# Performance work log

Hardware: AMD Instinct MI355X
Metric: run time of the kernel (lower is better)

The kernel has to match this reference:

```python
import jax, jax.numpy as jnp
import numpy as np

IN_DIM = 128
OUT_DIM = 128
D_MODEL = IN_DIM // 4        # mamba d_model = 32
D_STATE = 16
D_CONV = 4
EXPAND = 2
D_INNER = EXPAND * D_MODEL   # 64
DT_RANK = (D_MODEL + 15) // 16  # ceil(d_model/16) = 2
N_MIXERS = 3                 # shared + 2 experts (stacked on leading axis)
B, DD, HH, WW = 2, 16, 16, 16


def setup_inputs() -> dict:
    key = jax.random.key(0)
    ks = jax.random.split(key, 12)
    rn = lambda k, s, sc=0.05: jax.random.normal(k, s, dtype=jnp.float32) * sc
    M = N_MIXERS
    return {
        "x": jax.random.normal(ks[0], (B, IN_DIM, DD, HH, WW), dtype=jnp.float32),
        "dataset_id": jax.random.randint(ks[1], (B,), 0, 2),
        "ln_g": jnp.ones((M, IN_DIM), jnp.float32),
        "ln_b": jnp.zeros((M, IN_DIM), jnp.float32),
        "in_w": rn(ks[2], (M, 2 * D_INNER, D_MODEL)),
        "conv_w": rn(ks[3], (M, D_INNER, D_CONV), 0.2),
        "conv_b": rn(ks[4], (M, D_INNER), 0.1),
        "xp_w": rn(ks[5], (M, DT_RANK + 2 * D_STATE, D_INNER)),
        "dt_w": rn(ks[6], (M, D_INNER, DT_RANK), 0.2),
        "dt_b": rn(ks[7], (M, D_INNER), 0.1),
        "A_log": jnp.broadcast_to(jnp.log(jnp.arange(1, D_STATE + 1, dtype=jnp.float32)), (M, D_INNER, D_STATE)) + jnp.zeros((M, D_INNER, D_STATE), jnp.float32),
        "Dp": jnp.ones((M, D_INNER), jnp.float32),
        "out_w": rn(ks[8], (M, D_MODEL, D_INNER)),
        "proj_w": rn(ks[9], (M, OUT_DIM, IN_DIM)),
        "proj_b": jnp.zeros((M, OUT_DIM), jnp.float32),
        "skip": jnp.ones((M,), jnp.float32),
    }


def layernorm(x, g, b, eps=1e-5):
    mu = jnp.mean(x, -1, keepdims=True)
    var = jnp.mean((x - mu) ** 2, -1, keepdims=True)
    return (x - mu) * jax.lax.rsqrt(var + eps) * g + b


def mamba(xp, p):
    # Standard Mamba block: in_proj -> causal depthwise conv1d -> selective scan -> SiLU gate -> out_proj
    # xp: (B, L, d_model)
    Bb, L, _ = xp.shape
    xz = jnp.einsum('bld,ed->ble', xp, p["in_w"])            # (B,L,2*d_inner)
    xi, z = jnp.split(xz, 2, axis=-1)
    conv = jax.lax.conv_general_dilated(xi.transpose(0, 2, 1), p["conv_w"][:, None, :], (1,), [(D_CONV - 1, 0)], feature_group_count=D_INNER)
    xi = jax.nn.silu(conv + p["conv_b"][None, :, None]).transpose(0, 2, 1)  # (B,L,d_inner)
    dbc = jnp.einsum('bld,ed->ble', xi, p["xp_w"])
    dt_low = dbc[..., :DT_RANK]
    Bm = dbc[..., DT_RANK:DT_RANK + D_STATE]
    Cm = dbc[..., DT_RANK + D_STATE:]
    delta = jax.nn.softplus(jnp.einsum('blr,dr->bld', dt_low, p["dt_w"]) + p["dt_b"])  # (B,L,d_inner)
    A = -jnp.exp(p["A_log"])                                  # (d_inner, d_state)

    def step(h, inp):
        xt, dt, Bt, Ct = inp                                  # (B,di),(B,di),(B,ds),(B,ds)
        dA = jnp.exp(dt[..., None] * A)                       # (B,d_inner,d_state)
        h = dA * h + (dt * xt)[..., None] * Bt[:, None, :]
        return h, jnp.einsum('bds,bs->bd', h, Ct)

    h0 = jnp.zeros((Bb, D_INNER, D_STATE), xp.dtype)
    xs = (xi.transpose(1, 0, 2), delta.transpose(1, 0, 2), Bm.transpose(1, 0, 2), Cm.transpose(1, 0, 2))
    _, ys = jax.lax.scan(step, h0, xs)
    y = ys.transpose(1, 0, 2) + p["Dp"] * xi
    y = y * jax.nn.silu(z)
    return jnp.einsum('ble,de->bld', y, p["out_w"])


def mixer(x, p):
    # PetaloMixer pom_module='full': LN -> 4-way channel chunk -> shared Mamba + skip -> concat -> LN -> Linear
    Bb, C, Dd, Hh, Ww = x.shape
    L = Dd * Hh * Ww
    xf = x.reshape(Bb, C, L).transpose(0, 2, 1)               # (B,L,C)
    xn = layernorm(xf, p["ln_g"], p["ln_b"])
    parts = jnp.stack(jnp.split(xn, 4, axis=-1), 0)           # (4,B,L,d_model)
    outs = jax.vmap(lambda q: mamba(q, p))(parts) + p["skip"] * parts
    xm = jnp.concatenate([outs[i] for i in range(4)], -1)     # (B,L,C)
    xm = layernorm(xm, p["ln_g"], p["ln_b"])                  # same LayerNorm reused, as in torch code
    xpj = jnp.einsum('blc,oc->blo', xm, p["proj_w"]) + p["proj_b"]
    return xpj.transpose(0, 2, 1).reshape(Bb, OUT_DIM, Dd, Hh, Ww)


def _forward(x, dataset_id, params):
    shared = mixer(x, {k: v[0] for k, v in params.items()})
    # experts: compute both over full batch (vectorized), then per-sample select by dataset_id
    eouts = jax.vmap(lambda p: mixer(x, p))({k: v[1:] for k, v in params.items()})  # (2,B,out,D,H,W)
    ids = jnp.minimum(dataset_id, N_MIXERS - 2)               # clamp: min(m, n_experts-1)
    expert_out = eouts[ids, jnp.arange(x.shape[0])]
    return shared + expert_out                                # Dropout3d(p=0.2) is identity in eval mode


def reference(x, dataset_id, ln_g, ln_b, in_w, conv_w, conv_b, xp_w, dt_w, dt_b, A_log, Dp, out_w, proj_w, proj_b, skip):
    params = dict(ln_g=ln_g, ln_b=ln_b, in_w=in_w, conv_w=conv_w, conv_b=conv_b, xp_w=xp_w, dt_w=dt_w, dt_b=dt_b, A_log=A_log, Dp=Dp, out_w=out_w, proj_w=proj_w, proj_b=proj_b, skip=skip)
    return _forward(x, dataset_id, params)
```

## Files before the change

### kernel.cpp

```cpp
#include <hip/hip_runtime.h>
#include <math.h>

#define LSEQ 4096
#define CIN  128
#define DI   64
#define NS   16
#define NP   4
#define NJ   4
#define NSEQ 16
#define NC   128
#define LC   32
#define LOG2E 1.44269504f
#define LN2   0.6931471806f

__device__ __forceinline__ int mixer_of(const int* did, int j){
  if((j&1)==0) return 0;
  int d = did[j>>1];
  return 1 + (d < 1 ? d : 1);
}
__device__ __forceinline__ float fexp2(float x){ return __builtin_amdgcn_exp2f(x); }
__device__ __forceinline__ float silu_f(float x){
  return x*__builtin_amdgcn_rcpf(1.f + fexp2(-x*LOG2E));
}
__device__ __forceinline__ float softplus_f(float x){
  return x>20.f ? x : LN2*__builtin_amdgcn_logf(1.f + fexp2(x*LOG2E));
}

__global__ __launch_bounds__(256) void k12_fused(
  const float* __restrict__ x, const int* __restrict__ did,
  const float* __restrict__ ln_g, const float* __restrict__ ln_b,
  const float* __restrict__ in_w,
  const float* __restrict__ conv_w, const float* __restrict__ conv_b,
  const float* __restrict__ xp_w, const float* __restrict__ dt_w, const float* __restrict__ dt_b,
  const float* __restrict__ A_log,
  float* __restrict__ xnb, float* __restrict__ zb, float* __restrict__ dxb,
  float* __restrict__ bmb, float* __restrict__ cmb,
  float* __restrict__ pb, float* __restrict__ eb)
{
  const int seq = blockIdx.y, j = seq>>2, q = seq&3, b = j>>1;
  const int chunk = blockIdx.x, l0 = chunk*32;
  const int m = mixer_of(did, j);
  const int t = threadIdx.x, d = t&63, r = t>>6;

  __shared__ float s_x[36*132];
  __shared__ float s_xn[36][36];
  __shared__ float s_xzf[35][64];
  __shared__ float s_bS[32][16];
  __shared__ float s_dbc[32][2];
  __shared__ float s_cwT[4][64];
  __shared__ float s_xpw01[2][64];
  __shared__ float s_cb[64], s_dtw[128], s_dtb[64];
  __shared__ float s_mu[36], s_rs[36];
  float* s_xi = s_x;
  float* s_dl = s_x + 2048;

  for(int idx=t; idx<1152; idx+=256){
    int c = idx/9, f = idx - c*9;
    int l = l0 - 4 + f*4;
    float4 v;
    if(l >= 0) v = *(const float4*)(x + ((size_t)b*CIN + c)*LSEQ + l);
    else       v = make_float4(0.f,0.f,0.f,0.f);
    s_x[(f*4+0)*132 + c] = v.x;
    s_x[(f*4+1)*132 + c] = v.y;
    s_x[(f*4+2)*132 + c] = v.z;
    s_x[(f*4+3)*132 + c] = v.w;
  }
  float wreg_in[32];
  {
    const float4* wp = (const float4*)(in_w + (size_t)m*4096 + (size_t)(t&127)*32);
    #pragma unroll
    for(int i=0;i<8;i++){
      float4 v = wp[i];
      wreg_in[i*4+0]=v.x; wreg_in[i*4+1]=v.y; wreg_in[i*4+2]=v.z; wreg_in[i*4+3]=v.w;
    }
  }
  { int k=t>>6, dd=t&63; s_cwT[k][dd]=conv_w[m*256+dd*4+k]; }
  if(t<64){ s_cb[t]=conv_b[m*64+t]; s_dtb[t]=dt_b[m*64+t]; }
  if(t<128){ s_dtw[t]=dt_w[m*128+t]; s_xpw01[t>>6][t&63]=xp_w[m*2176 + t]; }
  __syncthreads();

  {
    const int lane=t&63, g=lane&7, lw=lane>>3;
    {
      int row = r*8 + lw;
      const float4* xr4 = (const float4*)(s_x + row*132 + g*16);
      float sum=0.f, vs=0.f;
      #pragma unroll
      for(int k=0;k<4;k++){
        float4 v = xr4[k];
        sum += (v.x+v.y)+(v.z+v.w);
        vs  += v.x*v.x + v.y*v.y + v.z*v.z + v.w*v.w;
      }
      sum += __shfl_xor(sum,1); vs += __shfl_xor(vs,1);
      sum += __shfl_xor(sum,2); vs += __shfl_xor(vs,2);
      sum += __shfl_xor(sum,4); vs += __shfl_xor(vs,4);
      float mu  = sum*(1.f/128.f);
      float var = fmaxf(vs*(1.f/128.f) - mu*mu, 0.f);
      if(g==0){ s_mu[row]=mu; s_rs[row]=rsqrtf(var+1e-5f); }
    }
    if(r==0 && lw<4){
      int row = 32 + lw;
      const float4* xr4 = (const float4*)(s_x + row*132 + g*16);
      float sum=0.f, vs=0.f;
      #pragma unroll
      for(int k=0;k<4;k++){
        float4 v = xr4[k];
        sum += (v.x+v.y)+(v.z+v.w);
        vs  += v.x*v.x + v.y*v.y + v.z*v.z + v.w*v.w;
      }
      sum += __shfl_xor(sum,1); vs += __shfl_xor(vs,1);
      sum += __shfl_xor(sum,2); vs += __shfl_xor(vs,2);
      sum += __shfl_xor(sum,4); vs += __shfl_xor(vs,4);
      float mu  = sum*(1.f/128.f);
      float var = fmaxf(vs*(1.f/128.f) - mu*mu, 0.f);
      if(g==0){ s_mu[row]=mu; s_rs[row]=rsqrtf(var+1e-5f); }
    }
  }
  __syncthreads();

  for(int idx=t; idx<1120; idx+=256){
    int row = (idx>>5) + 1, cc = idx&31;
    float xv = s_x[row*132 + q*32 + cc];
    float xn = (xv - s_mu[row])*s_rs[row]*ln_g[m*128 + q*32+cc] + ln_b[m*128 + q*32+cc];
    s_xn[row][cc] = xn;
    if(row>=4) xnb[((size_t)j*LSEQ + l0+row-4)*128 + q*32+cc] = xn;
  }
  __syncthreads();

  {
    const int e = t&127, hh = t>>7;
    if(e < 64){
      int r0 = 1 + hh*18, r1 = hh ? 36 : 19;
      for(int row=r0; row<r1; ++row){
        const float4* xr4 = (const float4*)(&s_xn[row][0]);
        float acc=0.f;
        #pragma unroll
        for(int k4=0;k4<8;k4++){
          float4 xv = xr4[k4];
          acc += xv.x*wreg_in[k4*4+0] + xv.y*wreg_in[k4*4+1]
               + xv.z*wreg_in[k4*4+2] + xv.w*wreg_in[k4*4+3];
        }
        if(chunk==0 && row<4) acc = 0.f;
        s_xzf[row-1][e] = acc;
      }
    } else {
      int r0 = 4 + hh*16, r1 = r0 + 16;
      for(int row=r0; row<r1; ++row){
        const float4* xr4 = (const float4*)(&s_xn[row][0]);
        float acc=0.f;
        #pragma unroll
        for(int k4=0;k4<8;k4++){
          float4 xv = xr4[k4];
          acc += xv.x*wreg_in[k4*4+0] + xv.y*wreg_in[k4*4+1]
               + xv.z*wreg_in[k4*4+2] + xv.w*wreg_in[k4*4+3];
        }
        zb[((size_t)seq*LSEQ + l0+row-4)*64 + (e-64)] = acc;
      }
    }
  }
  const int o2 = t&31, rg = t>>5;
  float wreg[64];
  {
    const float4* wp = (const float4*)(xp_w + (size_t)m*2176 + (size_t)(2+o2)*64);
    #pragma unroll
    for(int k4=0;k4<16;k4++){
      float4 v = wp[k4];
      wreg[k4*4+0]=v.x; wreg[k4*4+1]=v.y; wreg[k4*4+2]=v.z; wreg[k4*4+3]=v.w;
    }
  }
  __syncthreads();

  float xir[8];
  {
    float lz[11];
    #pragma unroll
    for(int i=0;i<11;i++) lz[i] = s_xzf[r*8+i][d];
    float cw0=s_cwT[0][d], cw1=s_cwT[1][d], cw2=s_cwT[2][d], cw3=s_cwT[3][d], cb=s_cb[d];
    #pragma unroll
    for(int i=0;i<8;i++){
      float xc = cb + lz[i]*cw0 + lz[i+1]*cw1 + lz[i+2]*cw2 + lz[i+3]*cw3;
      xir[i] = silu_f(xc);
      s_xi[(r*8+i)*64 + d] = xir[i];
    }
  }

  {
    float pr[8];
    #pragma unroll
    for(int i=0;i<8;i++){
      float p0 = xir[i]*s_xpw01[0][d];
      float p1 = xir[i]*s_xpw01[1][d];
      float q0 = p0 + __shfl_xor(p0,1);
      float q1 = p1 + __shfl_xor(p1,1);
      pr[i] = (d&1) ? q1 : q0;
    }
    #pragma unroll
    for(int off=2; off<64; off<<=1){
      #pragma unroll
      for(int i=0;i<8;i++) pr[i] += __shfl_xor(pr[i], off);
    }
    if(d<2){
      #pragma unroll
      for(int i=0;i<8;i++) s_dbc[r*8+i][d] = pr[i];
    }
  }
  __syncthreads();

  {
    float w0=s_dtw[d*2], w1=s_dtw[d*2+1], bb=s_dtb[d];
    #pragma unroll
    for(int i=0;i<8;i++){
      int ll=r*8+i;
      float dtv = s_dbc[ll][0]*w0 + s_dbc[ll][1]*w1 + bb;
      float dlv = softplus_f(dtv);
      s_dl[ll*64 + d] = dlv;
      *(float2*)(dxb + ((size_t)seq*LSEQ + l0+ll)*128 + d*2) = make_float2(dlv, xir[i]);
    }
  }

  {
    #pragma unroll
    for(int ip=0; ip<2; ip++){
      int ll = rg*4 + ip*2;
      const float4* xa=(const float4*)(s_xi + ll*64);
      const float4* xb=(const float4*)(s_xi + (ll+1)*64);
      float a0=0.f,a1=0.f,b0=0.f,b1=0.f;
      #pragma unroll
      for(int k=0;k<16;k+=2){
        float4 u=xa[k], u2=xa[k+1], v=xb[k], v2=xb[k+1];
        a0 += u.x *wreg[4*k+0]+u.y *wreg[4*k+1]+u.z *wreg[4*k+2]+u.w *wreg[4*k+3];
        a1 += u2.x*wreg[4*k+4]+u2.y*wreg[4*k+5]+u2.z*wreg[4*k+6]+u2.w*wreg[4*k+7];
        b0 += v.x *wreg[4*k+0]+v.y *wreg[4*k+1]+v.z *wreg[4*k+2]+v.w *wreg[4*k+3];
        b1 += v2.x*wreg[4*k+4]+v2.y*wreg[4*k+5]+v2.z*wreg[4*k+6]+v2.w*wreg[4*k+7];
      }
      float A=a0+a1, Bv=b0+b1;
      if(o2<16){
        s_bS[ll][o2]=A; s_bS[ll+1][o2]=Bv;
        bmb[((size_t)seq*LSEQ + l0+ll  )*16 + o2]=A;
        bmb[((size_t)seq*LSEQ + l0+ll+1)*16 + o2]=Bv;
      } else {
        cmb[((size_t)seq*LSEQ + l0+ll  )*16 + o2-16]=A;
        cmb[((size_t)seq*LSEQ + l0+ll+1)*16 + o2-16]=Bv;
      }
    }
  }
  __syncthreads();

  {
    const int sq = r;
    float as_q[4], as0;
    {
      const float* ap = A_log + (size_t)m*1024 + d*16;
      as0 = -expf(ap[0])*LOG2E;
      #pragma unroll
      for(int k=0;k<4;k++) as_q[k] = -expf(ap[sq*4+k])*LOG2E;
    }
    bool stl = true;
    #pragma unroll
    for(int k=0;k<4;k++){ float ex=(float)(sq*4+k+1)*as0; stl = stl && (fabsf(as_q[k]-ex) <= 1e-4f*fabsf(ex)); }
    const bool structured = (__ballot(stl) == ~0ull);

    float E[4] = {0.f,0.f,0.f,0.f};
    float Sdl = 0.f;

    #define PSTEPF(i_, P0CODE) { \
      float dl = s_dl[(i_)*64 + d]; \
      float u  = dl * s_xi[(i_)*64 + d]; \
      Sdl += dl; \
      const float4 bv = *(const float4*)(&s_bS[i_][sq*4]); \
      float qv = fexp2(dl*as0); \
      float q2 = qv*qv; float q4 = q2*q2; (void)q2; (void)q4; \
      float p0 = (P0CODE); \
      float p1 = p0*qv, p2 = p1*qv, p3 = p2*qv; \
      E[0]=fmaf(p0,E[0],u*bv.x); E[1]=fmaf(p1,E[1],u*bv.y); \
      E[2]=fmaf(p2,E[2],u*bv.z); E[3]=fmaf(p3,E[3],u*bv.w); }

    #define PSTEPG(i_) { \
      float dl = s_dl[(i_)*64 + d]; \
      float u  = dl * s_xi[(i_)*64 + d]; \
      Sdl += dl; \
      const float4 bv = *(const float4*)(&s_bS[i_][sq*4]); \
      float p_[4]; \
      _Pragma("unroll") for(int k=0;k<4;k++) p_[k]=fexp2(dl*as_q[k]); \
      E[0]=fmaf(p_[0],E[0],u*bv.x); E[1]=fmaf(p_[1],E[1],u*bv.y); \
      E[2]=fmaf(p_[2],E[2],u*bv.z); E[3]=fmaf(p_[3],E[3],u*bv.w); }

    if(structured){
      if(sq==0){
        #pragma unroll 4
        for(int i=0;i<LC;i++){ PSTEPF(i, qv) }
      } else if(sq==1){
        #pragma unroll 4
        for(int i=0;i<LC;i++){ PSTEPF(i, q4*qv) }
      } else if(sq==2){
        #pragma unroll 4
        for(int i=0;i<LC;i++){ PSTEPF(i, (q4*q4)*qv) }
      } else {
        #pragma unroll 4
        for(int i=0;i<LC;i++){ PSTEPF(i, ((q4*q4)*q4)*qv) }
      }
    } else {
      #pragma unroll 4
      for(int i=0;i<LC;i++){ PSTEPG(i) }
    }
    #undef PSTEPF
    #undef PSTEPG

    size_t oo=(((size_t)seq*NC+chunk)*64+d)*16 + sq*4;
    *(float4*)(pb+oo) = make_float4(fexp2(Sdl*as_q[0]),fexp2(Sdl*as_q[1]),
                                    fexp2(Sdl*as_q[2]),fexp2(Sdl*as_q[3]));
    *(float4*)(eb+oo) = make_float4(E[0],E[1],E[2],E[3]);
  }
}

__global__ __launch_bounds__(256) void k3b_combine(
  float* p_hs, const float* __restrict__ eb)
{
  const int seq=blockIdx.y, q=blockIdx.x, t=threadIdx.x;
  const size_t elem = (size_t)q*256+t;
  #define OFF(c_) (((size_t)seq*NC+(c_))*1024 + elem)
  float pA[16],eA[16],pB[16],eB[16];
  #pragma unroll
  for(int k=0;k<16;k++){ pA[k]=p_hs[OFF(k)]; eA[k]=eb[OFF(k)]; }
  float h=0.f;
  for(int bt=0; bt<8; bt+=2){
    if(bt+1<8){
      #pragma unroll
      for(int k=0;k<16;k++){ pB[k]=p_hs[OFF((bt+1)*16+k)]; eB[k]=eb[OFF((bt+1)*16+k)]; }
    }
    #pragma unroll
    for(int k=0;k<16;k++){ p_hs[OFF(bt*16+k)]=h; h=fmaf(pA[k],h,eA[k]); }
    if(bt+2<8){
      #pragma unroll
      for(int k=0;k<16;k++){ pA[k]=p_hs[OFF((bt+2)*16+k)]; eA[k]=eb[OFF((bt+2)*16+k)]; }
    }
    #pragma unroll
    for(int k=0;k<16;k++){ p_hs[OFF((bt+1)*16+k)]=h; h=fmaf(pB[k],h,eB[k]); }
  }
  #undef OFF
}

__global__ __launch_bounds__(256) void k3c4_scan_outproj(
  const int* __restrict__ did, const float* __restrict__ A_log, const float* __restrict__ Dp,
  const float* __restrict__ dxb,
  const float* __restrict__ bmb, const float* __restrict__ cmb,
  const float* __restrict__ zb, const float* __restrict__ hsb,
  const float* __restrict__ out_w, const float* __restrict__ skipv,
  const float* __restrict__ xnb, float* __restrict__ xmb)
{
  const int seq=blockIdx.y, j=seq>>2, p=seq&3, t=threadIdx.x;
  const int wave=t>>6, d=t&63;
  const int cl=wave>>1, sh=wave&1, sh8=sh*8;
  const int chunk=blockIdx.x*2+cl;
  const int l0=blockIdx.x*2*LC;
  const int m=mixer_of(did,j);
  __shared__ float s_b[2*LC*NS];
  __shared__ float s_c[2*LC*NS];
  __shared__ float s_y0[64*64];
  __shared__ float s_y1[64*64];
  {
    const float4* bsrc=(const float4*)(bmb + ((size_t)seq*LSEQ + l0)*NS);
    const float4* csrc=(const float4*)(cmb + ((size_t)seq*LSEQ + l0)*NS);
    ((float4*)s_b)[t]=bsrc[t];
    ((float4*)s_c)[t]=csrc[t];
  }
  float as_h[8], as0;
  {
    const float* ap = A_log + (size_t)m*1024 + d*16;
    as0 = -expf(ap[0])*LOG2E;
    #pragma unroll
    for(int k=0;k<8;k++) as_h[k] = -expf(ap[sh8+k])*LOG2E;
  }
  bool stl = true;
  #pragma unroll
  for(int k=0;k<8;k++){ float ex=(float)(sh8+k+1)*as0; stl = stl && (fabsf(as_h[k]-ex) <= 1e-4f*fabsf(ex)); }
  const bool structured = (__ballot(stl) == ~0ull);

  const float dpv2 = (sh==0) ? Dp[m*64+d] : 0.f;
  float h[8];
  {
    const float4* hp=(const float4*)(hsb + (((size_t)seq*NC+chunk)*64+d)*16 + sh8);
    float4 v0=hp[0], v1=hp[1];
    h[0]=v0.x; h[1]=v0.y; h[2]=v0.z; h[3]=v0.w;
    h[4]=v1.x; h[5]=v1.y; h[6]=v1.z; h[7]=v1.w;
  }
  const float2* dxp=(const float2*)(dxb + ((size_t)seq*LSEQ + (size_t)chunk*LC)*128);
  float* s_yw = sh ? s_y1 : s_y0;
  __syncthreads();

  #define CSTEPF(i_, dx_, P0CODE) { \
    float dl=dx_.x, xv=dx_.y; float u=dl*xv; \
    const float4* bq=(const float4*)(s_b + cl*(LC*NS) + (i_)*NS + sh8); \
    const float4* cq=(const float4*)(s_c + cl*(LC*NS) + (i_)*NS + sh8); \
    float4 b0=bq[0],b1=bq[1],c0=cq[0],c1=cq[1]; \
    float bb[8]={b0.x,b0.y,b0.z,b0.w, b1.x,b1.y,b1.z,b1.w}; \
    float cc2[8]={c0.x,c0.y,c0.z,c0.w, c1.x,c1.y,c1.z,c1.w}; \
    float qv=fexp2(dl*as0); \
    float q2=qv*qv; float q4=q2*q2; (void)q2; (void)q4; \
    float pz[8]; pz[0]=(P0CODE); \
    _Pragma("unroll") for(int k=1;k<8;k++) pz[k]=pz[k-1]*qv; \
    float ya=0.f, yb2=0.f; \
    _Pragma("unroll") for(int k=0;k<8;k++){ \
      h[k]=fmaf(pz[k],h[k],u*bb[k]); \
      float hv=h[k]*cc2[k]; \
      if(k&1) yb2+=hv; else ya+=hv; } \
    float y=ya+yb2; y=fmaf(dpv2,xv,y); \
    s_yw[(cl*LC+(i_))*64 + d]=y; }

  #define CSTEPG(i_, dx_) { \
    float dl=dx_.x, xv=dx_.y; float u=dl*xv; \
    const float4* bq=(const float4*)(s_b + cl*(LC*NS) + (i_)*NS + sh8); \
    const float4* cq=(const float4*)(s_c + cl*(LC*NS) + (i_)*NS + sh8); \
    float4 b0=bq[0],b1=bq[1],c0=cq[0],c1=cq[1]; \
    float bb[8]={b0.x,b0.y,b0.z,b0.w, b1.x,b1.y,b1.z,b1.w}; \
    float cc2[8]={c0.x,c0.y,c0.z,c0.w, c1.x,c1.y,c1.z,c1.w}; \
    float pz[8]; \
    _Pragma("unroll") for(int k=0;k<8;k++) pz[k]=fexp2(dl*as_h[k]); \
    float ya=0.f, yb2=0.f; \
    _Pragma("unroll") for(int k=0;k<8;k++){ \
      h[k]=fmaf(pz[k],h[k],u*bb[k]); \
      float hv=h[k]*cc2[k]; \
      if(k&1) yb2+=hv; else ya+=hv; } \
    float y=ya+yb2; y=fmaf(dpv2,xv,y); \
    s_yw[(cl*LC+(i_))*64 + d]=y; }

  #define CLOOPF(P0CODE) { \
    float2 dxw[4]; \
    _Pragma("unroll") for(int k=0;k<4;k++) dxw[k]=dxp[k*64+d]; \
    for(int ii=0;ii<LC;ii+=4){ \
      float2 c0w=dxw[0],c1w=dxw[1],c2w=dxw[2],c3w=dxw[3]; \
      if(ii+4<LC){ _Pragma("unroll") for(int k=0;k<4;k++) dxw[k]=dxp[(ii+4+k)*64+d]; } \
      CSTEPF(ii+0,c0w,P0CODE); CSTEPF(ii+1,c1w,P0CODE); \
      CSTEPF(ii+2,c2w,P0CODE); CSTEPF(ii+3,c3w,P0CODE); } }

  if(structured){
    if(sh==0){ CLOOPF(qv) }
    else     { CLOOPF((q4*q4)*qv) }
  } else {
    float2 dxw[4];
    #pragma unroll
    for(int k=0;k<4;k++) dxw[k]=dxp[k*64+d];
    for(int ii=0;ii<LC;ii+=4){
      float2 c0w=dxw[0],c1w=dxw[1],c2w=dxw[2],c3w=dxw[3];
      if(ii+4<LC){
        #pragma unroll
        for(int k=0;k<4;k++) dxw[k]=dxp[(ii+4+k)*64+d];
      }
      CSTEPG(ii+0,c0w); CSTEPG(ii+1,c1w); CSTEPG(ii+2,c2w); CSTEPG(ii+3,c3w);
    }
  }
  #undef CLOOPF
  #undef CSTEPF
  #undef CSTEPG

  __syncthreads();
  {
    const float* zp = zb + ((size_t)seq*LSEQ + l0)*64;
    #pragma unroll
    for(int it=0; it<16; ++it){
      int idx = t + it*256;
      float ysum = s_y0[idx] + s_y1[idx];
      s_y0[idx] = ysum * silu_f(zp[idx]);
    }
  }
  const int o=t&31, grp=t>>5;
  float wreg[64];
  {
    const float4* wp=(const float4*)(out_w + (size_t)m*2048 + (size_t)o*64);
    #pragma unroll
    for(int k4=0;k4<16;k4++){
      float4 v=wp[k4];
      wreg[k4*4+0]=v.x; wreg[k4*4+1]=v.y; wreg[k4*4+2]=v.z; wreg[k4*4+3]=v.w;
    }
  }
  const float sk=skipv[m];
  __syncthreads();
  for(int ll=grp; ll<64; ll+=8){
    const float4* ya=(const float4*)&s_y0[ll*64];
    float a0=0.f,a1=0.f;
    #pragma unroll
    for(int k=0;k<16;k+=2){
      float4 u=ya[k], u2=ya[k+1];
      a0 += u.x *wreg[4*k+0]+u.y *wreg[4*k+1]+u.z *wreg[4*k+2]+u.w *wreg[4*k+3];
      a1 += u2.x*wreg[4*k+4]+u2.y*wreg[4*k+5]+u2.z*wreg[4*k+6]+u2.w*wreg[4*k+7];
    }
    size_t xidx=((size_t)j*LSEQ + l0+ll)*128 + p*32 + o;
    xmb[xidx]=(a0+a1) + sk*xnb[xidx];
  }
}

__global__ __launch_bounds__(256) void k5_ln2_proj(
  const int* __restrict__ did, const float* __restrict__ ln_g, const float* __restrict__ ln_b,
  const float* __restrict__ proj_w, const float* __restrict__ proj_b,
  const float* __restrict__ xmb, float* __restrict__ out)
{
  const int b=blockIdx.y, l0=blockIdx.x*8, t=threadIdx.x;
  const int eh = t>>7, local = t&127;
  const int j = 2*b+eh;
  const int m = mixer_of(did, j);
  __shared__ float s_xn[2][8][132];
  __shared__ float s_comb[8][132];
  __shared__ float s_murs[2][8][2];

  for(int idx=local; idx<1024; idx+=128){
    int ll=idx>>7, c=idx&127;
    s_xn[eh][ll][c] = xmb[((size_t)j*LSEQ + l0+ll)*128 + c];
  }
  __syncthreads();
  if(((t>>6)&1)==0){
    const int lane = t&63;
    const int g = lane&7, ll = lane>>3;
    float sum=0.f, vs=0.f;
    const float4* xr4 = (const float4*)(&s_xn[eh][ll][g*16]);
    #pragma unroll
    for(int k=0;k<4;k++){
      float4 v = xr4[k];
      sum += (v.x+v.y)+(v.z+v.w);
      vs  += v.x*v.x + v.y*v.y + v.z*v.z + v.w*v.w;
    }
    sum += __shfl_xor(sum,1); vs += __shfl_xor(vs,1);
    sum += __shfl_xor(sum,2); vs += __shfl_xor(vs,2);
    sum += __shfl_xor(sum,4); vs += __shfl_xor(vs,4);
    float mu  = sum*(1.f/128.f);
    float var = fmaxf(vs*(1.f/128.f) - mu*mu, 0.f);
    if(g==0){ s_murs[eh][ll][0]=mu; s_murs[eh][ll][1]=rsqrtf(var+1e-5f); }
  }
  __syncthreads();
  for(int idx=local; idx<1024; idx+=128){
    int ll=idx>>7, c=idx&127;
    float xn=(s_xn[eh][ll][c]-s_murs[eh][ll][0])*s_murs[eh][ll][1]*ln_g[m*128+c]+ln_b[m*128+c];
    s_xn[eh][ll][c]=xn;
  }
  __syncthreads();
  float acc[8];
  #pragma unroll
  for(int ll=0;ll<8;ll++) acc[ll]=0.f;
  {
    const float4* pw4 = (const float4*)(proj_w + (size_t)m*16384 + (size_t)local*128);
    #pragma unroll 4
    for(int c4=0;c4<32;c4++){
      float4 w = pw4[c4];
      int c = c4*4;
      #pragma unroll
      for(int ll=0;ll<8;ll++){
        acc[ll] += w.x*s_xn[eh][ll][c] + w.y*s_xn[eh][ll][c+1]
                 + w.z*s_xn[eh][ll][c+2] + w.w*s_xn[eh][ll][c+3];
      }
    }
  }
  float pb_v = proj_b[m*128+local];
  if(eh==0){
    #pragma unroll
    for(int ll=0;ll<8;ll++) s_comb[ll][local]=acc[ll]+pb_v;
  }
  __syncthreads();
  if(eh==1){
    #pragma unroll
    for(int ll=0;ll<8;ll++) s_comb[ll][local]+=acc[ll]+pb_v;
  }
  __syncthreads();
  for(int idx=t; idx<1024; idx+=256){
    int o=idx>>3, ll=idx&7;
    out[((size_t)b*128+o)*LSEQ + l0+ll] = s_comb[ll][o];
  }
}

extern "C" void kernel_launch(void* const* d_in, const int* in_sizes, int n_in,
                              void* d_out, int out_size, void* d_ws, size_t ws_size,
                              hipStream_t stream) {
  const float* x      = (const float*)d_in[0];
  const int*   did    = (const int*)d_in[1];
  const float* ln_g   = (const float*)d_in[2];
  const float* ln_b   = (const float*)d_in[3];
  const float* in_w   = (const float*)d_in[4];
  const float* conv_w = (const float*)d_in[5];
  const float* conv_b = (const float*)d_in[6];
  const float* xp_w   = (const float*)d_in[7];
  const float* dt_w   = (const float*)d_in[8];
  const float* dt_b   = (const float*)d_in[9];
  const float* A_log  = (const float*)d_in[10];
  const float* Dp     = (const float*)d_in[11];
  const float* out_w  = (const float*)d_in[12];
  const float* proj_w = (const float*)d_in[13];
  const float* proj_b = (const float*)d_in[14];
  const float* skipv  = (const float*)d_in[15];
  float* out = (float*)d_out;
  float* ws  = (float*)d_ws;

  float* xnb = ws;
  float* zb  = xnb + (size_t)NJ*LSEQ*128;
  float* dxb = zb  + (size_t)NSEQ*LSEQ*64;
  float* bmb = dxb + (size_t)NSEQ*LSEQ*128;
  float* cmb = bmb + (size_t)NSEQ*LSEQ*16;
  float* xmb = cmb + (size_t)NSEQ*LSEQ*16;
  float* pb  = xmb + (size_t)NJ*LSEQ*128;
  float* eb  = pb  + (size_t)NSEQ*NC*1024;
  float* hsb = pb;

  hipLaunchKernelGGL(k12_fused, dim3(NC,NSEQ), dim3(256), 0, stream,
                     x,did,ln_g,ln_b,in_w,conv_w,conv_b,xp_w,dt_w,dt_b,A_log,
                     xnb,zb,dxb,bmb,cmb,pb,eb);
  hipLaunchKernelGGL(k3b_combine, dim3(4,NSEQ), dim3(256), 0, stream, pb,eb);
  hipLaunchKernelGGL(k3c4_scan_outproj, dim3(NC/2,NSEQ), dim3(256), 0, stream,
                     did,A_log,Dp,dxb,bmb,cmb,zb,hsb,out_w,skipv,xnb,xmb);
  hipLaunchKernelGGL(k5_ln2_proj, dim3(LSEQ/8,2), dim3(256), 0, stream,
                     did,ln_g,ln_b,proj_w,proj_b,xmb,out);
}
```

Before: 119.1 us.

## Precompute LayerNorm stats in separate kernel, load only quarter channels per block

After: 140.4 us. +17.8%, slower.

```diff
diff --git a/kernel.cpp b/kernel.cpp
--- a/kernel.cpp
+++ b/kernel.cpp
@@ -26,8 +26,31 @@
   return x>20.f ? x : LN2*__builtin_amdgcn_logf(1.f + fexp2(x*LOG2E));
 }
 
+__global__ __launch_bounds__(256) void k0_stats(
+  const float* __restrict__ x, float* __restrict__ murs)
+{
+  const int b = blockIdx.y, t = threadIdx.x;
+  const int li = t&63, cg = t>>6;
+  const int l = blockIdx.x*64 + li;
+  __shared__ float s_sum[4][64], s_vs[4][64];
+  float sum=0.f, vs=0.f;
+  const float* xp = x + ((size_t)b*CIN + cg*32)*LSEQ + l;
+  #pragma unroll 8
+  for(int c=0;c<32;c++){ float v = xp[(size_t)c*LSEQ]; sum+=v; vs+=v*v; }
+  s_sum[cg][li]=sum; s_vs[cg][li]=vs;
+  __syncthreads();
+  if(cg==0){
+    float S = s_sum[0][li]+s_sum[1][li]+s_sum[2][li]+s_sum[3][li];
+    float V = s_vs[0][li]+s_vs[1][li]+s_vs[2][li]+s_vs[3][li];
+    float mu = S*(1.f/128.f);
+    float var = fmaxf(V*(1.f/128.f)-mu*mu, 0.f);
+    *(float2*)(murs + ((size_t)b*LSEQ + l)*2) = make_float2(mu, rsqrtf(var+1e-5f));
+  }
+}
+
 __global__ __launch_bounds__(256) void k12_fused(
   const float* __restrict__ x, const int* __restrict__ did,
+  const float* __restrict__ murs,
   const float* __restrict__ ln_g, const float* __restrict__ ln_b,
   const float* __restrict__ in_w,
   const float* __restrict__ conv_w, const float* __restrict__ conv_b,
@@ -42,28 +65,29 @@
   const int m = mixer_of(did, j);
   const int t = threadIdx.x, d = t&63, r = t>>6;
 
-  __shared__ float s_x[36*132];
   __shared__ float s_xn[36][36];
-  __shared__ float s_xzf[35][64];
+  __shared__ float s_xzf[35*64];
+  __shared__ float s_xi[32*64];
   __shared__ float s_bS[32][16];
   __shared__ float s_dbc[32][2];
   __shared__ float s_cwT[4][64];
   __shared__ float s_xpw01[2][64];
   __shared__ float s_cb[64], s_dtw[128], s_dtb[64];
   __shared__ float s_mu[36], s_rs[36];
-  float* s_xi = s_x;
-  float* s_dl = s_x + 2048;
-
-  for(int idx=t; idx<1152; idx+=256){
+  float* s_dl = s_xzf;
+
+  for(int idx=t; idx<288; idx+=256){
     int c = idx/9, f = idx - c*9;
     int l = l0 - 4 + f*4;
     float4 v;
-    if(l >= 0) v = *(const float4*)(x + ((size_t)b*CIN + c)*LSEQ + l);
+    if(l >= 0) v = *(const float4*)(x + ((size_t)b*CIN + q*32 + c)*LSEQ + l);
     else       v = make_float4(0.f,0.f,0.f,0.f);
-    s_x[(f*4+0)*132 + c] = v.x;
-    s_x[(f*4+1)*132 + c] = v.y;
-    s_x[(f*4+2)*132 + c] = v.z;
-    s_x[(f*4+3)*132 + c] = v.w;
+    s_xn[f*4+0][c]=v.x; s_xn[f*4+1][c]=v.y; s_xn[f*4+2][c]=v.z; s_xn[f*4+3][c]=v.w;
+  }
+  if(t<36){
+    int l = l0 - 4 + t; if(l<0) l=0;
+    float2 v = *(const float2*)(murs + ((size_t)b*LSEQ + l)*2);
+    s_mu[t]=v.x; s_rs[t]=v.y;
   }
   float wreg_in[32];
   {
@@ -77,50 +101,21 @@
   { int k=t>>6, dd=t&63; s_cwT[k][dd]=conv_w[m*256+dd*4+k]; }
   if(t<64){ s_cb[t]=conv_b[m*64+t]; s_dtb[t]=dt_b[m*64+t]; }
   if(t<128){ s_dtw[t]=dt_w[m*128+t]; s_xpw01[t>>6][t&63]=xp_w[m*2176 + t]; }
-  __syncthreads();
-
-  {
-    const int lane=t&63, g=lane&7, lw=lane>>3;
-    {
-      int row = r*8 + lw;
-      const float4* xr4 = (const float4*)(s_x + row*132 + g*16);
-      float sum=0.f, vs=0.f;
-      #pragma unroll
-      for(int k=0;k<4;k++){
-        float4 v = xr4[k];
-        sum += (v.x+v.y)+(v.z+v.w);
-        vs  += v.x*v.x + v.y*v.y + v.z*v.z + v.w*v.w;
-      }
-      sum += __shfl_xor(sum,1); vs += __shfl_xor(vs,1);
-      sum += __shfl_xor(sum,2); vs += __shfl_xor(vs,2);
-      sum += __shfl_xor(sum,4); vs += __shfl_xor(vs,4);
-      float mu  = sum*(1.f/128.f);
-      float var = fmaxf(vs*(1.f/128.f) - mu*mu, 0.f);
-      if(g==0){ s_mu[row]=mu; s_rs[row]=rsqrtf(var+1e-5f); }
-    }
-    if(r==0 && lw<4){
-      int row = 32 + lw;
-      const float4* xr4 = (const float4*)(s_x + row*132 + g*16);
-      float sum=0.f, vs=0.f;
-      #pragma unroll
-      for(int k=0;k<4;k++){
-        float4 v = xr4[k];
-        sum += (v.x+v.y)+(v.z+v.w);
-        vs  += v.x*v.x + v.y*v.y + v.z*v.z + v.w*v.w;
-      }
-      sum += __shfl_xor(sum,1); vs += __shfl_xor(vs,1);
-      sum += __shfl_xor(sum,2); vs += __shfl_xor(vs,2);
-      sum += __shfl_xor(sum,4); vs += __shfl_xor(vs,4);
-      float mu  = sum*(1.f/128.f);
-      float var = fmaxf(vs*(1.f/128.f) - mu*mu, 0.f);
-      if(g==0){ s_mu[row]=mu; s_rs[row]=rsqrtf(var+1e-5f); }
+  const int o2 = t&31, rg = t>>5;
+  float wreg[64];
+  {
+    const float4* wp = (const float4*)(xp_w + (size_t)m*2176 + (size_t)(2+o2)*64);
+    #pragma unroll
+    for(int k4=0;k4<16;k4++){
+      float4 v = wp[k4];
+      wreg[k4*4+0]=v.x; wreg[k4*4+1]=v.y; wreg[k4*4+2]=v.z; wreg[k4*4+3]=v.w;
     }
   }
   __syncthreads();
 
   for(int idx=t; idx<1120; idx+=256){
     int row = (idx>>5) + 1, cc = idx&31;
-    float xv = s_x[row*132 + q*32 + cc];
+    float xv = s_xn[row][cc];
     float xn = (xv - s_mu[row])*s_rs[row]*ln_g[m*128 + q*32+cc] + ln_b[m*128 + q*32+cc];
     s_xn[row][cc] = xn;
     if(row>=4) xnb[((size_t)j*LSEQ + l0+row-4)*128 + q*32+cc] = xn;
@@ -141,7 +136,7 @@
                + xv.z*wreg_in[k4*4+2] + xv.w*wreg_in[k4*4+3];
         }
         if(chunk==0 && row<4) acc = 0.f;
-        s_xzf[row-1][e] = acc;
+        s_xzf[(row-1)*64 + e] = acc;
       }
     } else {
       int r0 = 4 + hh*16, r1 = r0 + 16;
@@ -158,23 +153,13 @@
       }
     }
   }
-  const int o2 = t&31, rg = t>>5;
-  float wreg[64];
-  {
-    const float4* wp = (const float4*)(xp_w + (size_t)m*2176 + (size_t)(2+o2)*64);
-    #pragma unroll
-    for(int k4=0;k4<16;k4++){
-      float4 v = wp[k4];
-      wreg[k4*4+0]=v.x; wreg[k4*4+1]=v.y; wreg[k4*4+2]=v.z; wreg[k4*4+3]=v.w;
-    }
-  }
   __syncthreads();
 
   float xir[8];
   {
     float lz[11];
     #pragma unroll
-    for(int i=0;i<11;i++) lz[i] = s_xzf[r*8+i][d];
+    for(int i=0;i<11;i++) lz[i] = s_xzf[(r*8+i)*64 + d];
     float cw0=s_cwT[0][d], cw1=s_cwT[1][d], cw2=s_cwT[2][d], cw3=s_cwT[3][d], cb=s_cb[d];
     #pragma unroll
     for(int i=0;i<8;i++){
@@ -595,10 +580,12 @@
   float* xmb = cmb + (size_t)NSEQ*LSEQ*16;
   float* pb  = xmb + (size_t)NJ*LSEQ*128;
   float* eb  = pb  + (size_t)NSEQ*NC*1024;
+  float* murs= eb  + (size_t)NSEQ*NC*1024;
   float* hsb = pb;
 
+  hipLaunchKernelGGL(k0_stats, dim3(LSEQ/64,2), dim3(256), 0, stream, x, murs);
   hipLaunchKernelGGL(k12_fused, dim3(NC,NSEQ), dim3(256), 0, stream,
-                     x,did,ln_g,ln_b,in_w,conv_w,conv_b,xp_w,dt_w,dt_b,A_log,
+                     x,did,murs,ln_g,ln_b,in_w,conv_w,conv_b,xp_w,dt_w,dt_b,A_log,
                      xnb,zb,dxb,bmb,cmb,pb,eb);
   hipLaunchKernelGGL(k3b_combine, dim3(4,NSEQ), dim3(256), 0, stream, pb,eb);
   hipLaunchKernelGGL(k3c4_scan_outproj, dim3(NC/2,NSEQ), dim3(256), 0, stream,
```
